# Performance work log

Hardware: AMD Instinct MI355X
Metric: run time of the kernel (lower is better)

Reference implementation:

```python
import jax, jax.numpy as jnp
import numpy as np

EPS = 1e-12  # torch F.normalize eps

def _l2norm(v, axis):
    return v / jnp.maximum(jnp.linalg.norm(v, axis=axis, keepdims=True), EPS)

def setup_inputs() -> dict:
    key = jax.random.key(0)
    k1, k2, k3, k4 = jax.random.split(key, 4)
    n, K, d, H, W = 32, 64, 256, 64, 64
    x = jax.random.normal(k1, (n, d, H, W), dtype=jnp.float32)
    conv_w = jax.random.normal(k2, (K, d), dtype=jnp.float32) * 0.05
    conv_b = jax.random.normal(k3, (K,), dtype=jnp.float32) * 0.05
    centroids = jax.random.uniform(k4, (K, d), dtype=jnp.float32)
    return {"x": x, "conv_w": conv_w, "conv_b": conv_b, "centroids": centroids}

def reference(x, conv_w, conv_b, centroids):
    n, c, H, W = x.shape
    K = centroids.shape[0]
    # input L2 normalization over channel dim
    x = _l2norm(x, axis=1)
    x_flat = x.reshape(n, c, H * W)                      # [n, c, S]
    # 1x1 conv == matmul over channels, then softmax over clusters
    logits = jnp.einsum('kc,ncs->nks', conv_w, x_flat) + conv_b[None, :, None]
    a = jax.nn.softmax(logits, axis=1)                   # [n, K, S]
    # vlad[n,k,c] = sum_s a[n,k,s] * (x[n,c,s] - cent[k,c])
    #            = (a @ x^T) - cent * sum_s a   (GEMM reformulation)
    vlad = jnp.einsum('nks,ncs->nkc', a, x_flat)
    vlad = vlad - a.sum(axis=2)[:, :, None] * centroids[None, :, :]
    # intra-normalize per cluster, flatten, global L2 normalize
    vlad = _l2norm(vlad, axis=2)
    vlad = vlad.reshape(n, K * c)
    vlad = _l2norm(vlad, axis=1)
    return vlad
```

## Files before the change

### kernel.cpp

```cpp
#include <hip/hip_runtime.h>
#include <math.h>

#define NIMG 32
#define CDIM 256
#define KCL  64
#define SPIX 4096

__global__ __launch_bounds__(256) void k_wt(const float* __restrict__ w, float* __restrict__ wT) {
    int g = blockIdx.x * 256 + threadIdx.x;
    if (g < KCL * CDIM) {
        int k = g / CDIM, c = g % CDIM;
        wT[c * KCL + k] = w[g];
    }
}

__global__ __launch_bounds__(512, 4) void k_logits(const float* __restrict__ x,
                                                   const float* __restrict__ wT,
                                                   const float* __restrict__ b,
                                                   float* __restrict__ aT,
                                                   float* __restrict__ inv_norm,
                                                   float* __restrict__ asum_part) {
    int blk = blockIdx.x;
    int n = blk >> 4, ch = blk & 15;
    int tid = threadIdx.x;
    int kh = __builtin_amdgcn_readfirstlane(tid >> 8);
    int sl = tid & 255;
    int s = ch * 256 + sl;

    __shared__ float red[512];

    const float* xp = x + ((size_t)n * CDIM) * SPIX + s;
    const float* wbase = wT + kh * 32;

    float acc[32];
    #pragma unroll
    for (int i = 0; i < 32; i++) acc[i] = 0.f;
    float nrm = 0.f;

    for (int c = 0; c < CDIM; c++) {
        float xv = xp[(size_t)c * SPIX];
        nrm = fmaf(xv, xv, nrm);
        const float4* wc = (const float4*)(wbase + c * 64);
        #pragma unroll
        for (int j = 0; j < 8; j++) {
            float4 wv = wc[j];
            acc[4*j+0] = fmaf(wv.x, xv, acc[4*j+0]);
            acc[4*j+1] = fmaf(wv.y, xv, acc[4*j+1]);
            acc[4*j+2] = fmaf(wv.z, xv, acc[4*j+2]);
            acc[4*j+3] = fmaf(wv.w, xv, acc[4*j+3]);
        }
    }

    float invn = 1.0f / fmaxf(sqrtf(nrm), 1e-12f);
    if (kh == 0) inv_norm[n * SPIX + s] = invn;

    const float4* b4 = (const float4*)b + kh * 8;
    float m = -1e30f;
    #pragma unroll
    for (int j = 0; j < 8; j++) {
        float4 bv = b4[j];
        acc[4*j+0] = fmaf(acc[4*j+0], invn, bv.x);
        acc[4*j+1] = fmaf(acc[4*j+1], invn, bv.y);
        acc[4*j+2] = fmaf(acc[4*j+2], invn, bv.z);
        acc[4*j+3] = fmaf(acc[4*j+3], invn, bv.w);
    }
    #pragma unroll
    for (int i = 0; i < 32; i++) m = fmaxf(m, acc[i]);
    red[tid] = m;
    __syncthreads();
    m = fmaxf(red[sl], red[256 + sl]);
    float ssum = 0.f;
    #pragma unroll
    for (int i = 0; i < 32; i++) { float e = __expf(acc[i] - m); acc[i] = e; ssum += e; }
    __syncthreads();
    red[tid] = ssum;
    __syncthreads();
    float r = 1.0f / (red[sl] + red[256 + sl]);
    #pragma unroll
    for (int i = 0; i < 32; i++) acc[i] *= r;

    float4* ap = (float4*)(aT + ((size_t)(n * SPIX + s)) * KCL + kh * 32);
    #pragma unroll
    for (int j = 0; j < 8; j++) {
        float4 v; v.x = acc[4*j+0]; v.y = acc[4*j+1]; v.z = acc[4*j+2]; v.w = acc[4*j+3];
        ap[j] = v;
    }

    int wv = tid >> 6, lane = tid & 63;
    #pragma unroll
    for (int i = 0; i < 32; i++) {
        float v = acc[i];
        #pragma unroll
        for (int off = 32; off > 0; off >>= 1) v += __shfl_xor(v, off, 64);
        if (lane == 0) asum_part[(blk * 8 + wv) * 32 + i] = v;
    }
}

__global__ __launch_bounds__(512, 4) void k_vlad(const float* __restrict__ x,
                                                 const float* __restrict__ inv_norm,
                                                 const float* __restrict__ aT,
                                                 float* __restrict__ vlad_part) {
    int blk = blockIdx.x;
    int n = blk >> 4, g = blk & 15;
    int tid = threadIdx.x;
    int kh = __builtin_amdgcn_readfirstlane(tid >> 8);
    int c = tid & 255;

    __shared__ float xt[256 * 33];

    float acc[32];
    #pragma unroll
    for (int i = 0; i < 32; i++) acc[i] = 0.f;

    int sl = tid & 31;
    int cr = tid >> 5;

    for (int t = 0; t < 8; t++) {
        int s0 = g * 256 + t * 32;
        float invp = inv_norm[n * SPIX + s0 + sl];
        __syncthreads();
        #pragma unroll
        for (int i = 0; i < 16; i++) {
            int cc = cr + i * 16;
            xt[cc * 33 + sl] = x[((size_t)n * CDIM + cc) * SPIX + s0 + sl] * invp;
        }
        __syncthreads();

        const float* ab = aT + ((size_t)(n * SPIX + s0)) * KCL + kh * 32;
        for (int ss = 0; ss < 32; ss++) {
            float xn = xt[c * 33 + ss];
            const float4* ap = (const float4*)(ab + ss * 64);
            #pragma unroll
            for (int q = 0; q < 8; q++) {
                float4 a4 = ap[q];
                acc[4*q+0] = fmaf(a4.x, xn, acc[4*q+0]);
                acc[4*q+1] = fmaf(a4.y, xn, acc[4*q+1]);
                acc[4*q+2] = fmaf(a4.z, xn, acc[4*q+2]);
                acc[4*q+3] = fmaf(a4.w, xn, acc[4*q+3]);
            }
        }
    }
    float* vp = vlad_part + ((size_t)blk * KCL + kh * 32) * CDIM + c;
    #pragma unroll
    for (int i = 0; i < 32; i++) vp[(size_t)i * CDIM] = acc[i];
}

__global__ __launch_bounds__(256) void k_combine(const float* __restrict__ vlad_part,
                                                 const float* __restrict__ asum_part,
                                                 const float* __restrict__ cent,
                                                 float* __restrict__ out,
                                                 float* __restrict__ rs) {
    int blk = blockIdx.x;
    int n = blk >> 6, k = blk & 63;
    int c = threadIdx.x;
    float v = 0.f;
    for (int j = 0; j < 16; j++)
        v += vlad_part[(((size_t)(n * 16 + j)) * KCL + k) * CDIM + c];
    float as = 0.f;
    int kh = k >> 5, kj = k & 31;
    for (int j = 0; j < 16; j++)
        for (int q = 0; q < 4; q++)
            as += asum_part[(((n * 16 + j) * 8) + kh * 4 + q) * 32 + kj];
    v = fmaf(-as, cent[k * CDIM + c], v);

    float t = v * v;
    #pragma unroll
    for (int off = 32; off > 0; off >>= 1) t += __shfl_xor(t, off, 64);
    __shared__ float w4[4];
    int lane = threadIdx.x & 63, wid = threadIdx.x >> 6;
    if (lane == 0) w4[wid] = t;
    __syncthreads();
    float ss = w4[0] + w4[1] + w4[2] + w4[3];
    float inv = 1.0f / fmaxf(sqrtf(ss), 1e-12f);
    out[(size_t)blk * CDIM + c] = v * inv;
    if (threadIdx.x == 0) rs[blk] = ss * inv * inv;
}

__global__ __launch_bounds__(256) void k_gnorm(const float* __restrict__ rs,
                                               float* __restrict__ out) {
    int n = blockIdx.x >> 3, j = blockIdx.x & 7;
    float ss = 0.f;
    for (int k = 0; k < KCL; k++) ss += rs[n * KCL + k];
    float g = 1.0f / fmaxf(sqrtf(ss), 1e-12f);
    size_t base = (size_t)n * (KCL * CDIM) + j * 2048 + threadIdx.x;
    for (int i = 0; i < 8; i++) out[base + i * 256] *= g;
}

extern "C" void kernel_launch(void* const* d_in, const int* in_sizes, int n_in,
                              void* d_out, int out_size, void* d_ws, size_t ws_size,
                              hipStream_t stream) {
    const float* x    = (const float*)d_in[0];
    const float* w    = (const float*)d_in[1];
    const float* b    = (const float*)d_in[2];
    const float* cent = (const float*)d_in[3];
    float* out = (float*)d_out;

    float* ws = (float*)d_ws;
    float* wT        = ws;
    float* inv_norm  = wT + 16384;
    float* aT        = inv_norm + 131072;
    float* vlad_part = aT + 8388608;
    float* asum_part = vlad_part + 8388608;
    float* rs        = asum_part + 131072;

    k_wt<<<64, 256, 0, stream>>>(w, wT);
    k_logits<<<512, 512, 0, stream>>>(x, wT, b, aT, inv_norm, asum_part);
    k_vlad<<<512, 512, 0, stream>>>(x, inv_norm, aT, vlad_part);
    k_combine<<<2048, 256, 0, stream>>>(vlad_part, asum_part, cent, out, rs);
    k_gnorm<<<256, 256, 0, stream>>>(rs, out);
}
```

Baseline: 170.0 us.

## Stage x tiles in LDS with float4 loads in logits kernel

k_logits now loads x in 32-channel chunks with coalesced float4 global loads into shared memory, computing the per-pixel squared-norm partials during the load and reducing them across waves. Previously each of the two thread halves read x one scalar per channel straight from global memory, so every element was loaded twice. The weight loads are hoisted into eight explicit float4 registers per channel step. The change adds block-wide barriers per chunk and about 40KB of LDS, which may lower occupancy.

```diff
diff --git a/kernel.cpp b/kernel.cpp
--- a/kernel.cpp
+++ b/kernel.cpp
@@ -13,6 +13,24 @@
         wT[c * KCL + k] = w[g];
     }
 }
+
+#define WFMA32() \
+    acc[0]=fmaf(w0_.x,xv,acc[0]);   acc[1]=fmaf(w0_.y,xv,acc[1]); \
+    acc[2]=fmaf(w0_.z,xv,acc[2]);   acc[3]=fmaf(w0_.w,xv,acc[3]); \
+    acc[4]=fmaf(w1_.x,xv,acc[4]);   acc[5]=fmaf(w1_.y,xv,acc[5]); \
+    acc[6]=fmaf(w1_.z,xv,acc[6]);   acc[7]=fmaf(w1_.w,xv,acc[7]); \
+    acc[8]=fmaf(w2_.x,xv,acc[8]);   acc[9]=fmaf(w2_.y,xv,acc[9]); \
+    acc[10]=fmaf(w2_.z,xv,acc[10]); acc[11]=fmaf(w2_.w,xv,acc[11]); \
+    acc[12]=fmaf(w3_.x,xv,acc[12]); acc[13]=fmaf(w3_.y,xv,acc[13]); \
+    acc[14]=fmaf(w3_.z,xv,acc[14]); acc[15]=fmaf(w3_.w,xv,acc[15]); \
+    acc[16]=fmaf(w4_.x,xv,acc[16]); acc[17]=fmaf(w4_.y,xv,acc[17]); \
+    acc[18]=fmaf(w4_.z,xv,acc[18]); acc[19]=fmaf(w4_.w,xv,acc[19]); \
+    acc[20]=fmaf(w5_.x,xv,acc[20]); acc[21]=fmaf(w5_.y,xv,acc[21]); \
+    acc[22]=fmaf(w5_.z,xv,acc[22]); acc[23]=fmaf(w5_.w,xv,acc[23]); \
+    acc[24]=fmaf(w6_.x,xv,acc[24]); acc[25]=fmaf(w6_.y,xv,acc[25]); \
+    acc[26]=fmaf(w6_.z,xv,acc[26]); acc[27]=fmaf(w6_.w,xv,acc[27]); \
+    acc[28]=fmaf(w7_.x,xv,acc[28]); acc[29]=fmaf(w7_.y,xv,acc[29]); \
+    acc[30]=fmaf(w7_.z,xv,acc[30]); acc[31]=fmaf(w7_.w,xv,acc[31]);
 
 __global__ __launch_bounds__(512, 4) void k_logits(const float* __restrict__ x,
                                                    const float* __restrict__ wT,
@@ -21,78 +39,103 @@
                                                    float* __restrict__ inv_norm,
                                                    float* __restrict__ asum_part) {
     int blk = blockIdx.x;
-    int n = blk >> 4, ch = blk & 15;
+    int n = blk >> 4, g = blk & 15;
+    int s0 = g * 256;
     int tid = threadIdx.x;
-    int kh = __builtin_amdgcn_readfirstlane(tid >> 8);
+    int wv = tid >> 6, l = tid & 63;
     int sl = tid & 255;
-    int s = ch * 256 + sl;
-
-    __shared__ float red[512];
-
-    const float* xp = x + ((size_t)n * CDIM) * SPIX + s;
-    const float* wbase = wT + kh * 32;
+    int khu = __builtin_amdgcn_readfirstlane(tid >> 8);
+
+    __shared__ float xs[32 * 256];
+    __shared__ float4 red4[8 * 64];
+    __shared__ float redf[512];
+    __shared__ float invs[256];
 
     float acc[32];
     #pragma unroll
     for (int i = 0; i < 32; i++) acc[i] = 0.f;
-    float nrm = 0.f;
-
-    for (int c = 0; c < CDIM; c++) {
-        float xv = xp[(size_t)c * SPIX];
-        nrm = fmaf(xv, xv, nrm);
-        const float4* wc = (const float4*)(wbase + c * 64);
+    float4 sq = {0.f, 0.f, 0.f, 0.f};
+
+    int cst = tid >> 6;
+    int p4 = (tid & 63) * 4;
+
+    for (int t = 0; t < 8; t++) {
+        if (t) __syncthreads();
         #pragma unroll
-        for (int j = 0; j < 8; j++) {
-            float4 wv = wc[j];
-            acc[4*j+0] = fmaf(wv.x, xv, acc[4*j+0]);
-            acc[4*j+1] = fmaf(wv.y, xv, acc[4*j+1]);
-            acc[4*j+2] = fmaf(wv.z, xv, acc[4*j+2]);
-            acc[4*j+3] = fmaf(wv.w, xv, acc[4*j+3]);
-        }
-    }
-
-    float invn = 1.0f / fmaxf(sqrtf(nrm), 1e-12f);
-    if (kh == 0) inv_norm[n * SPIX + s] = invn;
-
-    const float4* b4 = (const float4*)b + kh * 8;
-    float m = -1e30f;
+        for (int i = 0; i < 4; i++) {
+            int c = cst + 8 * i;
+            float4 xq = *(const float4*)(x + ((size_t)(n * CDIM + t * 32 + c)) * SPIX + s0 + p4);
+            sq.x = fmaf(xq.x, xq.x, sq.x);
+            sq.y = fmaf(xq.y, xq.y, sq.y);
+            sq.z = fmaf(xq.z, xq.z, sq.z);
+            sq.w = fmaf(xq.w, xq.w, sq.w);
+            *(float4*)(xs + c * 256 + p4) = xq;
+        }
+        __syncthreads();
+        const float* wrow = wT + (size_t)(t * 32) * KCL + khu * 32;
+        #pragma unroll 8
+        for (int cc = 0; cc < 32; cc++) {
+            float xv = xs[cc * 256 + sl];
+            const float4* wp = (const float4*)(wrow + (size_t)cc * KCL);
+            float4 w0_=wp[0], w1_=wp[1], w2_=wp[2], w3_=wp[3];
+            float4 w4_=wp[4], w5_=wp[5], w6_=wp[6], w7_=wp[7];
+            WFMA32()
+        }
+    }
+
+    red4[wv * 64 + l] = sq;
+    __syncthreads();
+    float4 ssq = red4[l];
+    #pragma unroll
+    for (int i = 1; i < 8; i++) {
+        float4 t4 = red4[i * 64 + l];
+        ssq.x += t4.x; ssq.y += t4.y; ssq.z += t4.z; ssq.w += t4.w;
+    }
+    if (wv == 0) {
+        float4 invn;
+        invn.x = 1.f / fmaxf(sqrtf(ssq.x), 1e-12f);
+        invn.y = 1.f / fmaxf(sqrtf(ssq.y), 1e-12f);
+        invn.z = 1.f / fmaxf(sqrtf(ssq.z), 1e-12f);
+        invn.w = 1.f / fmaxf(sqrtf(ssq.w), 1e-12f);
+        *(float4*)(invs + 4 * l) = invn;
+        *(float4*)(inv_norm + (size_t)n * SPIX + s0 + 4 * l) = invn;
+    }
+    __syncthreads();
+    float invp = invs[sl];
+
+    const float* bb = b + khu * 32;
+    #pragma unroll
+    for (int i = 0; i < 32; i++) acc[i] = fmaf(acc[i], invp, bb[i]);
+
+    float m = acc[0];
+    #pragma unroll
+    for (int i = 1; i < 32; i++) m = fmaxf(m, acc[i]);
+    redf[tid] = m;
+    __syncthreads();
+    m = fmaxf(redf[sl], redf[256 + sl]);
+    float ssum = 0.f;
+    #pragma unroll
+    for (int i = 0; i < 32; i++) { float e = __expf(acc[i] - m); acc[i] = e; ssum += e; }
+    __syncthreads();
+    redf[tid] = ssum;
+    __syncthreads();
+    float r = 1.0f / (redf[sl] + redf[256 + sl]);
+    #pragma unroll
+    for (int i = 0; i < 32; i++) acc[i] *= r;
+
+    float4* ap = (float4*)(aT + ((size_t)(n * SPIX + s0 + sl)) * KCL + khu * 32);
     #pragma unroll
     for (int j = 0; j < 8; j++) {
-        float4 bv = b4[j];
-        acc[4*j+0] = fmaf(acc[4*j+0], invn, bv.x);
-        acc[4*j+1] = fmaf(acc[4*j+1], invn, bv.y);
-        acc[4*j+2] = fmaf(acc[4*j+2], invn, bv.z);
-        acc[4*j+3] = fmaf(acc[4*j+3], invn, bv.w);
-    }
-    #pragma unroll
-    for (int i = 0; i < 32; i++) m = fmaxf(m, acc[i]);
-    red[tid] = m;
-    __syncthreads();
-    m = fmaxf(red[sl], red[256 + sl]);
-    float ssum = 0.f;
-    #pragma unroll
-    for (int i = 0; i < 32; i++) { float e = __expf(acc[i] - m); acc[i] = e; ssum += e; }
-    __syncthreads();
-    red[tid] = ssum;
-    __syncthreads();
-    float r = 1.0f / (red[sl] + red[256 + sl]);
-    #pragma unroll
-    for (int i = 0; i < 32; i++) acc[i] *= r;
-
-    float4* ap = (float4*)(aT + ((size_t)(n * SPIX + s)) * KCL + kh * 32);
-    #pragma unroll
-    for (int j = 0; j < 8; j++) {
-        float4 v; v.x = acc[4*j+0]; v.y = acc[4*j+1]; v.z = acc[4*j+2]; v.w = acc[4*j+3];
+        float4 v = {acc[4*j+0], acc[4*j+1], acc[4*j+2], acc[4*j+3]};
         ap[j] = v;
     }
 
-    int wv = tid >> 6, lane = tid & 63;
     #pragma unroll
     for (int i = 0; i < 32; i++) {
         float v = acc[i];
         #pragma unroll
         for (int off = 32; off > 0; off >>= 1) v += __shfl_xor(v, off, 64);
-        if (lane == 0) asum_part[(blk * 8 + wv) * 32 + i] = v;
+        if (l == 0) asum_part[(blk * 8 + wv) * 32 + i] = v;
     }
 }
 
```

Result: slower. 185.3 us (+9.0%).
